# Kernel optimization log

Measured on AMD Instinct MI355X. Metric: run time of the kernel, lower is better.

## Reference

```python
import jax, jax.numpy as jnp
import numpy as np

HEADS = 8
DIM_HEAD = 64
NUM_MEM_KV = 4

def rmsnorm(x, g):
    # F.normalize(x, dim=1) * g * sqrt(C): L2-normalize over channel dim with eps clamp
    n = jnp.sqrt(jnp.sum(x * x, axis=1, keepdims=True))
    return x / jnp.maximum(n, 1e-12) * g * (x.shape[1] ** 0.5)

def setup_inputs() -> dict:
    key = jax.random.key(0)
    ks = jax.random.split(key, 7)
    b, c, h, w = 32, 512, 32, 32
    hidden = HEADS * DIM_HEAD
    x = jax.random.normal(ks[0], (b, c, h, w), jnp.float32)
    g_in = 1.0 + 0.02 * jax.random.normal(ks[1], (1, c, 1, 1), jnp.float32)
    w_qkv = jax.random.normal(ks[2], (3 * hidden, c), jnp.float32) * (c ** -0.5)
    mem_kv = jax.random.normal(ks[3], (2, HEADS, DIM_HEAD, NUM_MEM_KV), jnp.float32)
    w_out = jax.random.normal(ks[4], (c, hidden), jnp.float32) * (hidden ** -0.5)
    b_out = 0.01 * jax.random.normal(ks[5], (c,), jnp.float32)
    g_out = 1.0 + 0.02 * jax.random.normal(ks[6], (1, c, 1, 1), jnp.float32)
    return {"x": x, "g_in": g_in, "w_qkv": w_qkv, "mem_kv": mem_kv,
            "w_out": w_out, "b_out": b_out, "g_out": g_out}

def reference(x, g_in, w_qkv, mem_kv, w_out, b_out, g_out):
    b, c, h, w = x.shape
    scale = DIM_HEAD ** -0.5
    xn = rmsnorm(x, g_in)
    # 1x1 conv (no bias) == channel GEMM
    qkv = jnp.einsum('bchw,oc->bohw', xn, w_qkv)
    q, k, v = jnp.split(qkv, 3, axis=1)
    to_heads = lambda t: t.reshape(b, HEADS, DIM_HEAD, h * w)  # b (h c) x y -> b h c (xy)
    q, k, v = map(to_heads, (q, k, v))
    mk = jnp.broadcast_to(mem_kv[0], (b,) + mem_kv[0].shape)
    mv = jnp.broadcast_to(mem_kv[1], (b,) + mem_kv[1].shape)
    k = jnp.concatenate([mk, k], axis=-1)
    v = jnp.concatenate([mv, v], axis=-1)
    q = jax.nn.softmax(q, axis=-2) * scale   # softmax over feature dim d
    k = jax.nn.softmax(k, axis=-1)           # softmax over sequence dim n
    context = jnp.einsum('bhdn,bhen->bhde', k, v)
    out = jnp.einsum('bhde,bhdn->bhen', context, q)
    out = out.reshape(b, HEADS * DIM_HEAD, h, w)
    out = jnp.einsum('bchw,oc->bohw', out, w_out) + b_out[None, :, None, None]
    return rmsnorm(out, g_out)
```

## Files before the change

kernel.cpp:

```cpp
#include <hip/hip_runtime.h>
#include <hip/hip_bf16.h>


#define AS1 __attribute__((address_space(1)))
#define AS3 __attribute__((address_space(3)))

using short8 = __attribute__((ext_vector_type(8))) short;
using usht4  = __attribute__((ext_vector_type(4))) unsigned short;
using f32x4  = __attribute__((ext_vector_type(4))) float;

__device__ __forceinline__ unsigned short f2bf(float f) {
  unsigned int u = __float_as_uint(f);
  u += 0x7fffu + ((u >> 16) & 1u);
  return (unsigned short)(u >> 16);
}
__device__ __forceinline__ float bf2f(unsigned short s) {
  return __uint_as_float(((unsigned int)s) << 16);
}

__global__ __launch_bounds__(256, 4)
void norm_r(const float* __restrict__ X, float* __restrict__ R) {
  __shared__ float part[32][33];
  const int t = threadIdx.x;
  const int b = blockIdx.x >> 5;
  const int pos0 = (blockIdx.x & 31) * 32;
  const int pg = t & 7, cg = t >> 3;
  const float* xp = X + ((size_t)b * 512 + (size_t)cg * 16) * 1024 + pos0 + pg * 4;
  f32x4 s = {0.f, 0.f, 0.f, 0.f};
#pragma unroll
  for (int i = 0; i < 16; ++i) {
    f32x4 v = *(const f32x4*)(xp + (size_t)i * 1024);
    s += v * v;
  }
  part[cg][pg * 4 + 0] = s.x;
  part[cg][pg * 4 + 1] = s.y;
  part[cg][pg * 4 + 2] = s.z;
  part[cg][pg * 4 + 3] = s.w;
  __syncthreads();
  if (t < 32) {
    float tot = 0.f;
#pragma unroll
    for (int j = 0; j < 32; ++j) tot += part[j][t];
    R[(size_t)b * 1024 + pos0 + t] = 22.627416998f / fmaxf(sqrtf(tot), 1e-12f);
  }
}

__global__ __launch_bounds__(256, 4)
void norm_r_bf16(const unsigned short* __restrict__ X, float* __restrict__ R) {
  __shared__ float part[16][64];
  const int t = threadIdx.x;
  const int b = blockIdx.x >> 4;
  const int pos0 = (blockIdx.x & 15) * 64;
  const int pg = t & 15, cg = t >> 4;
  const unsigned short* xp =
      X + ((size_t)b * 512 + (size_t)cg * 32) * 1024 + pos0 + pg * 4;
  float s0 = 0.f, s1 = 0.f, s2 = 0.f, s3 = 0.f;
#pragma unroll 8
  for (int i = 0; i < 32; ++i) {
    usht4 v = *(const usht4*)(xp + (size_t)i * 1024);
    float a = bf2f(v.x), bb = bf2f(v.y), c = bf2f(v.z), d = bf2f(v.w);
    s0 += a * a; s1 += bb * bb; s2 += c * c; s3 += d * d;
  }
  part[cg][pg * 4 + 0] = s0;
  part[cg][pg * 4 + 1] = s1;
  part[cg][pg * 4 + 2] = s2;
  part[cg][pg * 4 + 3] = s3;
  __syncthreads();
  if (t < 64) {
    float tot = 0.f;
#pragma unroll
    for (int j = 0; j < 16; ++j) tot += part[j][t];
    R[(size_t)b * 1024 + pos0 + t] = 22.627416998f / fmaxf(sqrtf(tot), 1e-12f);
  }
}

__global__ __launch_bounds__(256, 4)
void xn_transpose(const float* __restrict__ X, const float* __restrict__ R,
                  unsigned short* __restrict__ XT) {
  __shared__ float tile[64][65];
  const int t = threadIdx.x;
  const int b = blockIdx.z, cb = blockIdx.y, pb = blockIdx.x;
  {
    const int p = t & 63, cg = t >> 6;
    const float r = R[(size_t)b * 1024 + pb * 64 + p];
    const float* xp = X + ((size_t)b * 512 + (size_t)(cb * 64 + cg * 16)) * 1024 + pb * 64 + p;
#pragma unroll
    for (int i = 0; i < 16; ++i)
      tile[cg * 16 + i][p] = xp[(size_t)i * 1024] * r;
  }
  __syncthreads();
#pragma unroll
  for (int k = 0; k < 2; ++k) {
    const int idx = k * 256 + t;
    const int p = idx >> 3, c8 = idx & 7;
    short8 v;
#pragma unroll
    for (int j = 0; j < 8; ++j) v[j] = (short)f2bf(tile[c8 * 8 + j][p]);
    *(short8*)(XT + ((size_t)b * 1024 + pb * 64 + p) * 512 + cb * 64 + c8 * 8) = v;
  }
}

__global__ __launch_bounds__(256, 4)
void cast_wqkv(const float* __restrict__ W, const float* __restrict__ g,
               unsigned short* __restrict__ O) {
  int i = blockIdx.x * 256 + threadIdx.x;
  O[i] = f2bf(W[i] * g[i & 511]);
}
__global__ __launch_bounds__(256, 4)
void cast_w(const float* __restrict__ W, unsigned short* __restrict__ O, int n) {
  int i = blockIdx.x * 256 + threadIdx.x;
  if (i < n) O[i] = f2bf(W[i]);
}

template <int MTOT, bool SPLIT3, bool BIAS>
__global__ __launch_bounds__(256, 2)
void gemm_bt(const unsigned short* __restrict__ A,
             const unsigned short* __restrict__ Ball,
             unsigned short* __restrict__ O0, unsigned short* __restrict__ O1,
             unsigned short* __restrict__ O2, const float* __restrict__ bias) {
  __shared__ char smem[34816];
  unsigned short* lA = (unsigned short*)smem;
  unsigned short* lB = lA + 128 * 64;
  const int t = threadIdx.x;
  const int lane = t & 63, w = t >> 6;
  const int wm = w >> 1, wn = w & 1;
  const int mt = blockIdx.x >> 3, nt = blockIdx.x & 7;
  const int b = blockIdx.y;
  const unsigned short* Ag = A + (size_t)(mt * 128) * 512;
  const unsigned short* Bg = Ball + ((size_t)b * 1024 + (size_t)nt * 128) * 512;
  const int scol = ((lane & 7) ^ (lane >> 3)) * 8;
  f32x4 acc[4][4] = {};

  for (int kt = 0; kt < 8; ++kt) {
    const unsigned short* As = Ag + kt * 64 + scol;
    const unsigned short* Bs = Bg + kt * 64 + scol;
#pragma unroll
    for (int i = 0; i < 4; ++i) {
      const int r = w * 32 + i * 8 + (lane >> 3);
      __builtin_amdgcn_global_load_lds(
          (const AS1 unsigned int*)(As + (size_t)r * 512),
          (AS3 unsigned int*)(lA + (w * 32 + i * 8) * 64), 16, 0, 0);
      __builtin_amdgcn_global_load_lds(
          (const AS1 unsigned int*)(Bs + (size_t)r * 512),
          (AS3 unsigned int*)(lB + (w * 32 + i * 8) * 64), 16, 0, 0);
    }
    __syncthreads();
#pragma unroll
    for (int ks = 0; ks < 2; ++ks) {
      const int pch = ((ks * 4 + (lane >> 4)) ^ (lane & 7)) * 8;
      short8 af[4], bfv[4];
#pragma unroll
      for (int i = 0; i < 4; ++i)
        af[i] = *(const short8*)(lA + (wm * 64 + i * 16 + (lane & 15)) * 64 + pch);
#pragma unroll
      for (int j = 0; j < 4; ++j)
        bfv[j] = *(const short8*)(lB + (wn * 64 + j * 16 + (lane & 15)) * 64 + pch);
#pragma unroll
      for (int i = 0; i < 4; ++i)
#pragma unroll
        for (int j = 0; j < 4; ++j)
          acc[i][j] = __builtin_amdgcn_mfma_f32_16x16x32_bf16(af[i], bfv[j],
                                                              acc[i][j], 0, 0, 0);
    }
    __syncthreads();
  }

  unsigned short* Cst = (unsigned short*)smem;
#pragma unroll
  for (int i = 0; i < 4; ++i)
#pragma unroll
    for (int j = 0; j < 4; ++j)
#pragma unroll
      for (int r = 0; r < 4; ++r) {
        const int row = wm * 64 + i * 16 + (lane >> 4) * 4 + r;
        const int col = wn * 64 + j * 16 + (lane & 15);
        float v = acc[i][j][r];
        if (BIAS) v += bias[mt * 128 + row];
        Cst[row * 136 + col] = f2bf(v);
      }
  __syncthreads();
  unsigned short* Og;
  if (SPLIT3) {
    const int sec = mt >> 2;
    unsigned short* base = (sec == 0) ? O0 : ((sec == 1) ? O1 : O2);
    Og = base + ((size_t)b * 512 + (size_t)(mt & 3) * 128) * 1024 + (size_t)nt * 128;
  } else {
    Og = O0 + ((size_t)b * MTOT + (size_t)mt * 128) * 1024 + (size_t)nt * 128;
  }
#pragma unroll
  for (int k = 0; k < 8; ++k) {
    const int f = t + k * 256;
    const int row = f >> 4, c8 = f & 15;
    short8 v = *(const short8*)(Cst + row * 136 + c8 * 8);
    *(short8*)(Og + (size_t)row * 1024 + c8 * 8) = v;
  }
}

__global__ __launch_bounds__(256, 2)
void attn_kernel(const unsigned short* __restrict__ Qp,
                 const unsigned short* __restrict__ Kp,
                 const unsigned short* __restrict__ Vp,
                 const float* __restrict__ memkv,
                 unsigned short* __restrict__ outT) {
  __shared__ char smem[36608];
  unsigned short* bufA = (unsigned short*)smem;
  unsigned short* bufB = (unsigned short*)(smem + 9216);
  float* Pl   = (float*)(smem + 18432);
  float* Pc   = (float*)(smem + 18432);
  float* csS  = (float*)(smem + 21504);
  float* msum = (float*)(smem + 35072);
  float* rsI  = (float*)(smem + 36096);
  const int t = threadIdx.x;
  const int lane = t & 63, wave = t >> 6;
  const int b = blockIdx.x >> 3, h = blockIdx.x & 7;
  const size_t hb = ((size_t)b * 512 + (size_t)h * 64) * 1024;
  const unsigned short* Qg = Qp + hb;
  const unsigned short* Kg = Kp + hb;
  const unsigned short* Vg = Vp + hb;
  const float* mk = memkv + (size_t)h * 256;
  const float* mv = memkv + 2048 + (size_t)h * 256;

  float rsum[2] = {0.f, 0.f};
  f32x4 cacc[4] = {};

  for (int it = 0; it < 17; ++it) {
    if (it == 0) {
      const int d = t & 63, j = t >> 6;
      const float ev = __expf(mk[d * 4 + j]);
      msum[d * 4 + j] = ev;
      bufA[d * 72 + j] = f2bf(ev);
      bufB[d * 72 + j] = f2bf(mv[d * 4 + j]);
      for (int c2 = 4 + j; c2 < 64; c2 += 4) {
        bufA[d * 72 + c2] = 0;
        bufB[d * 72 + c2] = 0;
      }
    } else {
      const int c0 = (it - 1) * 64;
#pragma unroll
      for (int z = 0; z < 2; ++z) {
        const int d = z * 32 + (t >> 3), ch = t & 7;
        short8 kv = *(const short8*)(Kg + (size_t)d * 1024 + c0 + ch * 8);
        short8 pk;
        float ssum = 0.f;
#pragma unroll
        for (int j = 0; j < 8; ++j) {
          const float e = __expf(bf2f((unsigned short)kv[j]));
          ssum += e;
          pk[j] = (short)f2bf(e);
        }
        rsum[z] += ssum;
        *(short8*)(bufA + d * 72 + ch * 8) = pk;
        short8 vv = *(const short8*)(Vg + (size_t)d * 1024 + c0 + ch * 8);
        *(short8*)(bufB + d * 72 + ch * 8) = vv;
      }
    }
    __syncthreads();
#pragma unroll
    for (int ks = 0; ks < 2; ++ks) {
      short8 a = *(const short8*)(bufA + (wave * 16 + (lane & 15)) * 72 +
                                  ks * 32 + (lane >> 4) * 8);
#pragma unroll
      for (int et = 0; et < 4; ++et) {
        short8 bb = *(const short8*)(bufB + (et * 16 + (lane & 15)) * 72 +
                                     ks * 32 + (lane >> 4) * 8);
        cacc[et] = __builtin_amdgcn_mfma_f32_16x16x32_bf16(a, bb, cacc[et], 0, 0, 0);
      }
    }
    __syncthreads();
  }

  Pl[t]       = rsum[0];
  Pl[256 + t] = rsum[1];
  __syncthreads();
  if (t < 64) {
    float s = 0.f;
#pragma unroll
    for (int ch = 0; ch < 8; ++ch) s += Pl[t * 8 + ch];
    s += msum[t * 4] + msum[t * 4 + 1] + msum[t * 4 + 2] + msum[t * 4 + 3];
    rsI[t] = 1.0f / s;
  }
  __syncthreads();

  unsigned short* CT = bufB;
#pragma unroll
  for (int et = 0; et < 4; ++et)
#pragma unroll
    for (int r = 0; r < 4; ++r) {
      const int d = wave * 16 + (lane >> 4) * 4 + r;
      const int e = et * 16 + (lane & 15);
      CT[e * 72 + d] = f2bf(cacc[et][r] * rsI[d]);
    }
  __syncthreads();

  short8 a0 = *(const short8*)(CT + (wave * 16 + (lane & 15)) * 72 + (lane >> 4) * 8);
  short8 a1 = *(const short8*)(CT + (wave * 16 + (lane & 15)) * 72 + 32 + (lane >> 4) * 8);
  unsigned short* oBase = outT + (size_t)b * 1024 * 512 + h * 64;

  for (int pt = 0; pt < 16; ++pt) {
    {
      const int p = lane, dq = wave;
      float cp = 0.f;
#pragma unroll
      for (int i2 = 0; i2 < 8; ++i2) {
        const int d0 = dq * 16 + i2 * 2;
        const float e0 = __expf(bf2f(Qg[(size_t)d0 * 1024 + pt * 64 + p]));
        const float e1 = __expf(bf2f(Qg[(size_t)(d0 + 1) * 1024 + pt * 64 + p]));
        cp += e0 + e1;
        const unsigned int pk =
            (unsigned int)f2bf(e0) | ((unsigned int)f2bf(e1) << 16);
        *(unsigned int*)(bufA + p * 72 + d0) = pk;
      }
      Pc[dq * 64 + p] = cp;
    }
    __syncthreads();
    if (t < 64) csS[t] = 0.125f / (Pc[t] + Pc[64 + t] + Pc[128 + t] + Pc[192 + t]);
    __syncthreads();
#pragma unroll
    for (int ps = 0; ps < 4; ++ps) {
      f32x4 oc = {};
      short8 b0 = *(const short8*)(bufA + (ps * 16 + (lane & 15)) * 72 + (lane >> 4) * 8);
      short8 b1 = *(const short8*)(bufA + (ps * 16 + (lane & 15)) * 72 + 32 + (lane >> 4) * 8);
      oc = __builtin_amdgcn_mfma_f32_16x16x32_bf16(a0, b0, oc, 0, 0, 0);
      oc = __builtin_amdgcn_mfma_f32_16x16x32_bf16(a1, b1, oc, 0, 0, 0);
      const float cs = csS[ps * 16 + (lane & 15)];
      const unsigned long long pk =
          (unsigned long long)f2bf(oc[0] * cs) |
          ((unsigned long long)f2bf(oc[1] * cs) << 16) |
          ((unsigned long long)f2bf(oc[2] * cs) << 32) |
          ((unsigned long long)f2bf(oc[3] * cs) << 48);
      const int p = pt * 64 + ps * 16 + (lane & 15);
      *(unsigned long long*)(oBase + (size_t)p * 512 + wave * 16 + (lane >> 4) * 4) = pk;
    }
    __syncthreads();
  }
}

__global__ __launch_bounds__(256, 4)
void final_scale_bf16(const unsigned short* __restrict__ P,
                      const float* __restrict__ R, const float* __restrict__ G,
                      float* __restrict__ O) {
  const size_t f = ((size_t)blockIdx.x * 256 + threadIdx.x) * 4;
  const int p = (int)(f & 1023);
  const int c = (int)((f >> 10) & 511);
  const int b = (int)(f >> 19);
  usht4 v = *(const usht4*)(P + f);
  const f32x4 r = *(const f32x4*)(R + (size_t)b * 1024 + p);
  const float g = G[c];
  f32x4 o;
  o.x = bf2f(v.x) * r.x * g;
  o.y = bf2f(v.y) * r.y * g;
  o.z = bf2f(v.z) * r.z * g;
  o.w = bf2f(v.w) * r.w * g;
  *(f32x4*)(O + f) = o;
}

extern "C" void kernel_launch(void* const* d_in, const int* in_sizes, int n_in,
                              void* d_out, int out_size, void* d_ws, size_t ws_size,
                              hipStream_t stream) {
  (void)in_sizes; (void)n_in; (void)out_size; (void)ws_size;
  const float* x     = (const float*)d_in[0];
  const float* g_in  = (const float*)d_in[1];
  const float* w_qkv = (const float*)d_in[2];
  const float* memkv = (const float*)d_in[3];
  const float* w_out = (const float*)d_in[4];
  const float* b_out = (const float*)d_in[5];
  const float* g_out = (const float*)d_in[6];
  float* out = (float*)d_out;

  char* ws = (char*)d_ws;
  float* r1           = (float*)ws;
  float* r2           = (float*)(ws + 131072);
  unsigned short* wqb = (unsigned short*)(ws + 262144);
  unsigned short* wob = (unsigned short*)(ws + 1835008);
  unsigned short* xnT = (unsigned short*)(ws + 2359296);
  unsigned short* Qp  = (unsigned short*)(ws + 35913728);
  unsigned short* outT = xnT;
  unsigned short* pre  = Qp;
  unsigned short* Kp  = (unsigned short*)d_out;
  unsigned short* Vp  = (unsigned short*)d_out + 16777216;

  norm_r<<<1024, 256, 0, stream>>>(x, r1);
  xn_transpose<<<dim3(16, 8, 32), 256, 0, stream>>>(x, r1, xnT);
  cast_wqkv<<<3072, 256, 0, stream>>>(w_qkv, g_in, wqb);
  cast_w<<<1024, 256, 0, stream>>>(w_out, wob, 262144);
  gemm_bt<1536, true, false><<<dim3(96, 32), 256, 0, stream>>>(
      wqb, xnT, Qp, Kp, Vp, nullptr);
  attn_kernel<<<256, 256, 0, stream>>>(Qp, Kp, Vp, memkv, outT);
  gemm_bt<512, false, true><<<dim3(32, 32), 256, 0, stream>>>(
      wob, outT, pre, nullptr, nullptr, b_out);
  norm_r_bf16<<<512, 256, 0, stream>>>(pre, r2);
  final_scale_bf16<<<16384, 256, 0, stream>>>(pre, r2, g_out, out);
}
```

Baseline: 279.7 us.

## Rewrite GEMM with 256x256 tiles, 512 threads and a 4-stage LDS pipeline

The bf16 GEMM kernel moves from 128x128 tiles with 256 threads and synchronous single-buffered K steps to 256x256 tiles with 8 waves. It uses a 4-deep ring of LDS buffers with K-step 32, prefetching three stages ahead with vmcnt-based waits, and raises priority around the MFMA block. The epilogue now stages each wave's tile separately in LDS, dropping a block-wide barrier. The aim is to hide global-load latency and raise reuse per tile. In exchange, 128 KB of LDS per block and larger accumulators limit occupancy, and the QKV and output GEMMs now launch far fewer blocks (768 and 256), which may underfill the GPU for the smaller GEMM.

```diff
diff --git a/kernel.cpp b/kernel.cpp
--- a/kernel.cpp
+++ b/kernel.cpp
@@ -113,86 +113,103 @@
 }
 
 template <int MTOT, bool SPLIT3, bool BIAS>
-__global__ __launch_bounds__(256, 2)
+__global__ __launch_bounds__(512, 2)
 void gemm_bt(const unsigned short* __restrict__ A,
              const unsigned short* __restrict__ Ball,
              unsigned short* __restrict__ O0, unsigned short* __restrict__ O1,
              unsigned short* __restrict__ O2, const float* __restrict__ bias) {
-  __shared__ char smem[34816];
-  unsigned short* lA = (unsigned short*)smem;
-  unsigned short* lB = lA + 128 * 64;
+  __shared__ __align__(16) unsigned short smem[65536];
   const int t = threadIdx.x;
   const int lane = t & 63, w = t >> 6;
-  const int wm = w >> 1, wn = w & 1;
-  const int mt = blockIdx.x >> 3, nt = blockIdx.x & 7;
+  const int wm = w >> 2, wn = w & 3;
+  const int mt = blockIdx.x >> 2, nt = blockIdx.x & 3;
   const int b = blockIdx.y;
-  const unsigned short* Ag = A + (size_t)(mt * 128) * 512;
-  const unsigned short* Bg = Ball + ((size_t)b * 1024 + (size_t)nt * 128) * 512;
-  const int scol = ((lane & 7) ^ (lane >> 3)) * 8;
-  f32x4 acc[4][4] = {};
-
-  for (int kt = 0; kt < 8; ++kt) {
-    const unsigned short* As = Ag + kt * 64 + scol;
-    const unsigned short* Bs = Bg + kt * 64 + scol;
-#pragma unroll
-    for (int i = 0; i < 4; ++i) {
-      const int r = w * 32 + i * 8 + (lane >> 3);
+  const unsigned short* Ag = A + (size_t)(mt * 256) * 512;
+  const unsigned short* Bg = Ball + ((size_t)b * 1024 + (size_t)nt * 256) * 512;
+
+  const int r0 = t >> 2;
+  const int csrc = (t & 3) ^ ((r0 >> 1) & 3);
+  const unsigned short* As0 = Ag + (size_t)r0 * 512 + csrc * 8;
+  const unsigned short* Bs0 = Bg + (size_t)r0 * 512 + csrc * 8;
+
+  auto STAGE = [&](int kt) {
+    unsigned short* dst = smem + (kt & 3) * 16384 + w * 512;
+    const size_t ko = (size_t)kt * 32;
+#pragma unroll
+    for (int i = 0; i < 2; ++i) {
       __builtin_amdgcn_global_load_lds(
-          (const AS1 unsigned int*)(As + (size_t)r * 512),
-          (AS3 unsigned int*)(lA + (w * 32 + i * 8) * 64), 16, 0, 0);
+          (const AS1 unsigned int*)(As0 + ko + (size_t)i * 65536),
+          (AS3 unsigned int*)(dst + i * 4096), 16, 0, 0);
       __builtin_amdgcn_global_load_lds(
-          (const AS1 unsigned int*)(Bs + (size_t)r * 512),
-          (AS3 unsigned int*)(lB + (w * 32 + i * 8) * 64), 16, 0, 0);
-    }
-    __syncthreads();
-#pragma unroll
-    for (int ks = 0; ks < 2; ++ks) {
-      const int pch = ((ks * 4 + (lane >> 4)) ^ (lane & 7)) * 8;
-      short8 af[4], bfv[4];
-#pragma unroll
-      for (int i = 0; i < 4; ++i)
-        af[i] = *(const short8*)(lA + (wm * 64 + i * 16 + (lane & 15)) * 64 + pch);
+          (const AS1 unsigned int*)(Bs0 + ko + (size_t)i * 65536),
+          (AS3 unsigned int*)(dst + 8192 + i * 4096), 16, 0, 0);
+    }
+  };
+
+  f32x4 acc[8][4] = {};
+  const int fsw = (((lane >> 4) ^ ((lane >> 1) & 3)) << 3);
+  const int am = (lane & 15);
+
+  STAGE(0); STAGE(1); STAGE(2);
+#pragma unroll 1
+  for (int kt = 0; kt < 16; ++kt) {
+    asm volatile("s_waitcnt vmcnt(8)" ::: "memory");
+    __builtin_amdgcn_s_barrier();
+    asm volatile("" ::: "memory");
+    const unsigned short* lA = smem + (kt & 3) * 16384;
+    const unsigned short* lB = lA + 8192;
+    short8 af[8], bf[4];
+#pragma unroll
+    for (int i = 0; i < 8; ++i) {
+      const int row = wm * 128 + i * 16 + am;
+      af[i] = *(const short8*)(lA + row * 32 + fsw);
+    }
+#pragma unroll
+    for (int j = 0; j < 4; ++j) {
+      const int row = wn * 64 + j * 16 + am;
+      bf[j] = *(const short8*)(lB + row * 32 + fsw);
+    }
+    STAGE((kt + 3) & 15);
+    __builtin_amdgcn_s_setprio(1);
+#pragma unroll
+    for (int i = 0; i < 8; ++i)
 #pragma unroll
       for (int j = 0; j < 4; ++j)
-        bfv[j] = *(const short8*)(lB + (wn * 64 + j * 16 + (lane & 15)) * 64 + pch);
-#pragma unroll
-      for (int i = 0; i < 4; ++i)
-#pragma unroll
-        for (int j = 0; j < 4; ++j)
-          acc[i][j] = __builtin_amdgcn_mfma_f32_16x16x32_bf16(af[i], bfv[j],
-                                                              acc[i][j], 0, 0, 0);
-    }
-    __syncthreads();
-  }
-
-  unsigned short* Cst = (unsigned short*)smem;
-#pragma unroll
-  for (int i = 0; i < 4; ++i)
+        acc[i][j] = __builtin_amdgcn_mfma_f32_16x16x32_bf16(af[i], bf[j],
+                                                            acc[i][j], 0, 0, 0);
+    __builtin_amdgcn_s_setprio(0);
+  }
+
+  asm volatile("s_waitcnt vmcnt(0)" ::: "memory");
+  __syncthreads();
+  unsigned short* Cw = smem + w * 8192;
+#pragma unroll
+  for (int i = 0; i < 8; ++i)
 #pragma unroll
     for (int j = 0; j < 4; ++j)
 #pragma unroll
       for (int r = 0; r < 4; ++r) {
-        const int row = wm * 64 + i * 16 + (lane >> 4) * 4 + r;
-        const int col = wn * 64 + j * 16 + (lane & 15);
+        const int row = i * 16 + (lane >> 4) * 4 + r;
+        const int col = j * 16 + (lane & 15);
         float v = acc[i][j][r];
-        if (BIAS) v += bias[mt * 128 + row];
-        Cst[row * 136 + col] = f2bf(v);
+        if (BIAS) v += bias[mt * 256 + wm * 128 + row];
+        Cw[row * 64 + col] = f2bf(v);
       }
-  __syncthreads();
   unsigned short* Og;
   if (SPLIT3) {
-    const int sec = mt >> 2;
+    const int sec = mt >> 1;
     unsigned short* base = (sec == 0) ? O0 : ((sec == 1) ? O1 : O2);
-    Og = base + ((size_t)b * 512 + (size_t)(mt & 3) * 128) * 1024 + (size_t)nt * 128;
+    Og = base + ((size_t)b * 512 + (size_t)((mt & 1) * 256 + wm * 128)) * 1024 +
+         nt * 256 + wn * 64;
   } else {
-    Og = O0 + ((size_t)b * MTOT + (size_t)mt * 128) * 1024 + (size_t)nt * 128;
-  }
-#pragma unroll
-  for (int k = 0; k < 8; ++k) {
-    const int f = t + k * 256;
-    const int row = f >> 4, c8 = f & 15;
-    short8 v = *(const short8*)(Cst + row * 136 + c8 * 8);
-    *(short8*)(Og + (size_t)row * 1024 + c8 * 8) = v;
+    Og = O0 + ((size_t)b * MTOT + (size_t)(mt * 256 + wm * 128)) * 1024 +
+         nt * 256 + wn * 64;
+  }
+#pragma unroll
+  for (int p = 0; p < 16; ++p) {
+    const int row = p * 8 + (lane >> 3);
+    short8 v = *(const short8*)(Cw + row * 64 + (lane & 7) * 8);
+    *(short8*)(Og + (size_t)row * 1024 + (lane & 7) * 8) = v;
   }
 }
 
@@ -383,10 +400,10 @@
   xn_transpose<<<dim3(16, 8, 32), 256, 0, stream>>>(x, r1, xnT);
   cast_wqkv<<<3072, 256, 0, stream>>>(w_qkv, g_in, wqb);
   cast_w<<<1024, 256, 0, stream>>>(w_out, wob, 262144);
-  gemm_bt<1536, true, false><<<dim3(96, 32), 256, 0, stream>>>(
+  gemm_bt<1536, true, false><<<dim3(24, 32), 512, 0, stream>>>(
       wqb, xnT, Qp, Kp, Vp, nullptr);
   attn_kernel<<<256, 256, 0, stream>>>(Qp, Kp, Vp, memkv, outT);
-  gemm_bt<512, false, true><<<dim3(32, 32), 256, 0, stream>>>(
+  gemm_bt<512, false, true><<<dim3(8, 32), 512, 0, stream>>>(
       wob, outT, pre, nullptr, nullptr, b_out);
   norm_r_bf16<<<512, 256, 0, stream>>>(pre, r2);
   final_scale_bf16<<<16384, 256, 0, stream>>>(pre, r2, g_out, out);
```

New measurement: 273.4 us. 2.3% less time.

## Fuse input norm with transpose and output norm with final scale

Applied to the files above, without the earlier changes.

Merges the input sum-of-squares pass and the normalize-transpose pass into a single kernel that stages a 512x32 fp32 tile in shared memory. It also merges the output norm pass and the final scaling pass into one kernel holding a 512x64 bf16 tile. Each input and pre-activation tensor is then read from global memory once rather than twice, and two launches and the row-scale buffers go away. In exchange, the kernels use large shared-memory tiles, which lowers occupancy, and the output-side kernel runs fewer, heavier blocks.

```diff
diff --git a/kernel.cpp b/kernel.cpp
--- a/kernel.cpp
+++ b/kernel.cpp
@@ -7,6 +7,7 @@
 
 using short8 = __attribute__((ext_vector_type(8))) short;
 using usht4  = __attribute__((ext_vector_type(4))) unsigned short;
+using f32x2  = __attribute__((ext_vector_type(2))) float;
 using f32x4  = __attribute__((ext_vector_type(4))) float;
 
 __device__ __forceinline__ unsigned short f2bf(float f) {
@@ -18,85 +19,97 @@
   return __uint_as_float(((unsigned int)s) << 16);
 }
 
-__global__ __launch_bounds__(256, 4)
-void norm_r(const float* __restrict__ X, float* __restrict__ R) {
+__global__ __launch_bounds__(256, 2)
+void xnorm_t(const float* __restrict__ X, unsigned short* __restrict__ XT) {
+  __shared__ float tile[512][34];
   __shared__ float part[32][33];
+  __shared__ float rloc[32];
   const int t = threadIdx.x;
   const int b = blockIdx.x >> 5;
   const int pos0 = (blockIdx.x & 31) * 32;
-  const int pg = t & 7, cg = t >> 3;
-  const float* xp = X + ((size_t)b * 512 + (size_t)cg * 16) * 1024 + pos0 + pg * 4;
-  f32x4 s = {0.f, 0.f, 0.f, 0.f};
+  const int pr = t & 7, cr = t >> 3;
+  const float* xp = X + ((size_t)b * 512 + cr) * 1024 + pos0 + pr * 4;
+  f32x4 ssq = {0.f, 0.f, 0.f, 0.f};
 #pragma unroll
   for (int i = 0; i < 16; ++i) {
-    f32x4 v = *(const f32x4*)(xp + (size_t)i * 1024);
-    s += v * v;
-  }
-  part[cg][pg * 4 + 0] = s.x;
-  part[cg][pg * 4 + 1] = s.y;
-  part[cg][pg * 4 + 2] = s.z;
-  part[cg][pg * 4 + 3] = s.w;
+    f32x4 v = *(const f32x4*)(xp + (size_t)(i * 32) * 1024);
+    ssq += v * v;
+    f32x2 lo = {v.x, v.y}, hi = {v.z, v.w};
+    *(f32x2*)(&tile[i * 32 + cr][pr * 4]) = lo;
+    *(f32x2*)(&tile[i * 32 + cr][pr * 4 + 2]) = hi;
+  }
+  part[cr][pr * 4 + 0] = ssq.x;
+  part[cr][pr * 4 + 1] = ssq.y;
+  part[cr][pr * 4 + 2] = ssq.z;
+  part[cr][pr * 4 + 3] = ssq.w;
   __syncthreads();
   if (t < 32) {
     float tot = 0.f;
 #pragma unroll
     for (int j = 0; j < 32; ++j) tot += part[j][t];
-    R[(size_t)b * 1024 + pos0 + t] = 22.627416998f / fmaxf(sqrtf(tot), 1e-12f);
-  }
-}
-
-__global__ __launch_bounds__(256, 4)
-void norm_r_bf16(const unsigned short* __restrict__ X, float* __restrict__ R) {
-  __shared__ float part[16][64];
+    rloc[t] = 22.627416998f / fmaxf(sqrtf(tot), 1e-12f);
+  }
+  __syncthreads();
+#pragma unroll
+  for (int k = 0; k < 8; ++k) {
+    const int idx = k * 256 + t;
+    const int p = idx >> 6, c8 = idx & 63;
+    const float r = rloc[p];
+    short8 v;
+#pragma unroll
+    for (int j = 0; j < 8; ++j) v[j] = (short)f2bf(tile[c8 * 8 + j][p] * r);
+    *(short8*)(XT + ((size_t)b * 1024 + pos0 + p) * 512 + c8 * 8) = v;
+  }
+}
+
+__global__ __launch_bounds__(256, 2)
+void norm_scale(const unsigned short* __restrict__ P, const float* __restrict__ G,
+                float* __restrict__ O) {
+  __shared__ unsigned short tile[512][68];
+  __shared__ float part[2048];
   const int t = threadIdx.x;
   const int b = blockIdx.x >> 4;
   const int pos0 = (blockIdx.x & 15) * 64;
-  const int pg = t & 15, cg = t >> 4;
-  const unsigned short* xp =
-      X + ((size_t)b * 512 + (size_t)cg * 32) * 1024 + pos0 + pg * 4;
-  float s0 = 0.f, s1 = 0.f, s2 = 0.f, s3 = 0.f;
-#pragma unroll 8
-  for (int i = 0; i < 32; ++i) {
-    usht4 v = *(const usht4*)(xp + (size_t)i * 1024);
-    float a = bf2f(v.x), bb = bf2f(v.y), c = bf2f(v.z), d = bf2f(v.w);
-    s0 += a * a; s1 += bb * bb; s2 += c * c; s3 += d * d;
-  }
-  part[cg][pg * 4 + 0] = s0;
-  part[cg][pg * 4 + 1] = s1;
-  part[cg][pg * 4 + 2] = s2;
-  part[cg][pg * 4 + 3] = s3;
+  const int pg = t & 7, cr = t >> 3;
+  const unsigned short* pp = P + ((size_t)b * 512 + cr) * 1024 + pos0 + pg * 8;
+  float s[8] = {};
+#pragma unroll
+  for (int i = 0; i < 16; ++i) {
+    short8 v = *(const short8*)(pp + (size_t)(i * 32) * 1024);
+    usht4 lo = {(unsigned short)v[0], (unsigned short)v[1],
+                (unsigned short)v[2], (unsigned short)v[3]};
+    usht4 hi = {(unsigned short)v[4], (unsigned short)v[5],
+                (unsigned short)v[6], (unsigned short)v[7]};
+    *(usht4*)(&tile[i * 32 + cr][pg * 8]) = lo;
+    *(usht4*)(&tile[i * 32 + cr][pg * 8 + 4]) = hi;
+#pragma unroll
+    for (int j = 0; j < 8; ++j) {
+      const float f = bf2f((unsigned short)v[j]);
+      s[j] += f * f;
+    }
+  }
+#pragma unroll
+  for (int j = 0; j < 8; ++j) part[cr * 64 + pg * 8 + j] = s[j];
   __syncthreads();
   if (t < 64) {
     float tot = 0.f;
 #pragma unroll
-    for (int j = 0; j < 16; ++j) tot += part[j][t];
-    R[(size_t)b * 1024 + pos0 + t] = 22.627416998f / fmaxf(sqrtf(tot), 1e-12f);
-  }
-}
-
-__global__ __launch_bounds__(256, 4)
-void xn_transpose(const float* __restrict__ X, const float* __restrict__ R,
-                  unsigned short* __restrict__ XT) {
-  __shared__ float tile[64][65];
-  const int t = threadIdx.x;
-  const int b = blockIdx.z, cb = blockIdx.y, pb = blockIdx.x;
-  {
-    const int p = t & 63, cg = t >> 6;
-    const float r = R[(size_t)b * 1024 + pb * 64 + p];
-    const float* xp = X + ((size_t)b * 512 + (size_t)(cb * 64 + cg * 16)) * 1024 + pb * 64 + p;
-#pragma unroll
-    for (int i = 0; i < 16; ++i)
-      tile[cg * 16 + i][p] = xp[(size_t)i * 1024] * r;
-  }
-  __syncthreads();
-#pragma unroll
-  for (int k = 0; k < 2; ++k) {
+    for (int j = 0; j < 32; ++j) tot += part[j * 64 + t];
+    part[t] = 22.627416998f / fmaxf(sqrtf(tot), 1e-12f);
+  }
+  __syncthreads();
+#pragma unroll
+  for (int k = 0; k < 32; ++k) {
     const int idx = k * 256 + t;
-    const int p = idx >> 3, c8 = idx & 7;
-    short8 v;
-#pragma unroll
-    for (int j = 0; j < 8; ++j) v[j] = (short)f2bf(tile[c8 * 8 + j][p]);
-    *(short8*)(XT + ((size_t)b * 1024 + pb * 64 + p) * 512 + cb * 64 + c8 * 8) = v;
+    const int c = idx >> 4, p4 = idx & 15;
+    usht4 v = *(const usht4*)(&tile[c][p4 * 4]);
+    const float g = G[c];
+    f32x4 o;
+    o.x = bf2f(v.x) * part[p4 * 4 + 0] * g;
+    o.y = bf2f(v.y) * part[p4 * 4 + 1] * g;
+    o.z = bf2f(v.z) * part[p4 * 4 + 2] * g;
+    o.w = bf2f(v.w) * part[p4 * 4 + 3] * g;
+    *(f32x4*)(O + ((size_t)b * 512 + c) * 1024 + pos0 + p4 * 4) = o;
   }
 }
 
@@ -335,25 +348,6 @@
   }
 }
 
-__global__ __launch_bounds__(256, 4)
-void final_scale_bf16(const unsigned short* __restrict__ P,
-                      const float* __restrict__ R, const float* __restrict__ G,
-                      float* __restrict__ O) {
-  const size_t f = ((size_t)blockIdx.x * 256 + threadIdx.x) * 4;
-  const int p = (int)(f & 1023);
-  const int c = (int)((f >> 10) & 511);
-  const int b = (int)(f >> 19);
-  usht4 v = *(const usht4*)(P + f);
-  const f32x4 r = *(const f32x4*)(R + (size_t)b * 1024 + p);
-  const float g = G[c];
-  f32x4 o;
-  o.x = bf2f(v.x) * r.x * g;
-  o.y = bf2f(v.y) * r.y * g;
-  o.z = bf2f(v.z) * r.z * g;
-  o.w = bf2f(v.w) * r.w * g;
-  *(f32x4*)(O + f) = o;
-}
-
 extern "C" void kernel_launch(void* const* d_in, const int* in_sizes, int n_in,
                               void* d_out, int out_size, void* d_ws, size_t ws_size,
                               hipStream_t stream) {
@@ -368,8 +362,6 @@
   float* out = (float*)d_out;
 
   char* ws = (char*)d_ws;
-  float* r1           = (float*)ws;
-  float* r2           = (float*)(ws + 131072);
   unsigned short* wqb = (unsigned short*)(ws + 262144);
   unsigned short* wob = (unsigned short*)(ws + 1835008);
   unsigned short* xnT = (unsigned short*)(ws + 2359296);
@@ -379,8 +371,7 @@
   unsigned short* Kp  = (unsigned short*)d_out;
   unsigned short* Vp  = (unsigned short*)d_out + 16777216;
 
-  norm_r<<<1024, 256, 0, stream>>>(x, r1);
-  xn_transpose<<<dim3(16, 8, 32), 256, 0, stream>>>(x, r1, xnT);
+  xnorm_t<<<1024, 256, 0, stream>>>(x, xnT);
   cast_wqkv<<<3072, 256, 0, stream>>>(w_qkv, g_in, wqb);
   cast_w<<<1024, 256, 0, stream>>>(w_out, wob, 262144);
   gemm_bt<1536, true, false><<<dim3(96, 32), 256, 0, stream>>>(
@@ -388,6 +379,5 @@
   attn_kernel<<<256, 256, 0, stream>>>(Qp, Kp, Vp, memkv, outT);
   gemm_bt<512, false, true><<<dim3(32, 32), 256, 0, stream>>>(
       wob, outT, pre, nullptr, nullptr, b_out);
-  norm_r_bf16<<<512, 256, 0, stream>>>(pre, r2);
-  final_scale_bf16<<<16384, 256, 0, stream>>>(pre, r2, g_out, out);
-}
+  norm_scale<<<512, 256, 0, stream>>>(pre, g_out, out);
+}
```

After: 256.4 us. -8.3%, faster.
